# Performance work log

Hardware: AMD Instinct MI355X
Metric: run time of the kernel (lower is better)

The kernel has to match this reference:

```python
import jax, jax.numpy as jnp
import numpy as np

WIN = 7
SIGMA = 1.5
C1 = 0.01 ** 2
C2 = 0.03 ** 2


def _gaussian_window(channels):
    # 1D gaussian, normalized (matches pytorch_ssim.create_window)
    xs = np.arange(WIN, dtype=np.float32)
    g = np.exp(-((xs - WIN // 2) ** 2) / (2.0 * SIGMA ** 2))
    g = g / g.sum()
    w2d = np.outer(g, g).astype(np.float32)  # [7,7], sums to 1
    # depthwise kernel [C,1,7,7] (OIHW with feature_group_count=C)
    return jnp.asarray(np.tile(w2d[None, None], (channels, 1, 1, 1)))


def _dwconv(img, win, channels):
    # img: [N,C,H,W]; 'same' padding for odd window (pad=3)
    return jax.lax.conv_general_dilated(
        img, win, window_strides=(1, 1), padding=[(3, 3), (3, 3)],
        feature_group_count=channels,
        dimension_numbers=('NCHW', 'OIHW', 'NCHW'))


def _ssim(img1, img2):
    C = img1.shape[1]
    win = _gaussian_window(C).astype(img1.dtype)
    mu1 = _dwconv(img1, win, C)
    mu2 = _dwconv(img2, win, C)
    mu1_sq = mu1 * mu1
    mu2_sq = mu2 * mu2
    mu1_mu2 = mu1 * mu2
    sigma1_sq = _dwconv(img1 * img1, win, C) - mu1_sq
    sigma2_sq = _dwconv(img2 * img2, win, C) - mu2_sq
    sigma12 = _dwconv(img1 * img2, win, C) - mu1_mu2
    ssim_map = ((2.0 * mu1_mu2 + C1) * (2.0 * sigma12 + C2)) / (
        (mu1_sq + mu2_sq + C1) * (sigma1_sq + sigma2_sq + C2))
    return jnp.mean(ssim_map)  # size_average=True


def setup_inputs() -> dict:
    key = jax.random.key(0)
    k1, k2 = jax.random.split(key)
    B, T, C, H, W = 8, 8, 3, 256, 256
    x = jax.random.uniform(k1, (B, T, C, H, W), dtype=jnp.float32)
    y = jax.random.uniform(k2, (B, T, C, H, W), dtype=jnp.float32)
    return {"x": x, "y": y}


def reference(x, y):
    # flatten(0,1): [B,T,C,H,W] -> [B*T,C,H,W]
    x2 = x.reshape((-1,) + x.shape[2:])
    y2 = y.reshape((-1,) + y.shape[2:])
    return _ssim(x2, y2)
```

## Files before the change

### kernel.cpp

```cpp
#include <hip/hip_runtime.h>

#define IMG_H 256
#define IMG_W 256
#define TW 64
#define TH 16
#define SC 72

typedef float v2f __attribute__((ext_vector_type(2)));

__device__ __forceinline__ int rotc(int r, int c) { return (c & ~7) | ((c + r) & 7); }

#define G0 0.03663285f
#define G1 0.11128076f
#define G2 0.21674532f
#define G3 0.27068216f

__global__ __launch_bounds__(256) void ssim_tile_kernel(
    const float* __restrict__ x, const float* __restrict__ y,
    float* __restrict__ partial) {
    __shared__ float4 vs[TH][SC];
    __shared__ float  wsum[4];

    const int tid = threadIdx.x;
    const int bx = blockIdx.x, by = blockIdx.y, plane = blockIdx.z;
    const int r0 = by * TH, c0 = bx * TW;
    const size_t base = (size_t)plane * (IMG_H * IMG_W);
    const float g[7] = {G0, G1, G2, G3, G2, G1, G0};

    v2f g2[7];
    #pragma unroll
    for (int d = 0; d < 7; ++d) { g2[d].x = g[d]; g2[d].y = g[d]; }

    const bool fast = ((bx == 1) | (bx == 2)) & (by >= 1) & (by <= 14);

    auto vtask = [&](int a, int c) {
        const int gc = c0 - 4 + c;
        const int rstart = r0 - 3 + 4 * a;

        float xr[10], yr[10];
        if (fast) {
            const float* px = x + base + (size_t)rstart * IMG_W + gc;
            const float* py = y + base + (size_t)rstart * IMG_W + gc;
            #pragma unroll
            for (int t = 0; t < 10; ++t) {
                xr[t] = px[t * IMG_W];
                yr[t] = py[t * IMG_W];
            }
        } else {
            const bool ok_c = ((unsigned)gc < IMG_W);
            const int  gcc  = gc < 0 ? 0 : (gc > IMG_W - 1 ? IMG_W - 1 : gc);
            #pragma unroll
            for (int t = 0; t < 10; ++t) {
                const int gr  = rstart + t;
                const bool ok = ok_c & ((unsigned)gr < IMG_H);
                const int grc = gr < 0 ? 0 : (gr > IMG_H - 1 ? IMG_H - 1 : gr);
                const size_t idx = base + ((size_t)grc << 8) + gcc;
                float xv = x[idx], yv = y[idx];
                xr[t] = ok ? xv : 0.f;
                yr[t] = ok ? yv : 0.f;
            }
        }

        v2f aA[4], aB[4];
        #pragma unroll
        for (int o = 0; o < 4; ++o) { aA[o] = (v2f)0.f; aB[o] = (v2f)0.f; }

        #pragma unroll
        for (int t = 0; t < 10; ++t) {
            const float xv = xr[t], yv = yr[t];
            v2f ina; ina.x = xv; ina.y = yv;
            v2f inb; inb.x = fmaf(xv, xv, yv * yv); inb.y = xv * yv;
            #pragma unroll
            for (int o = 0; o < 4; ++o) {
                const int dy = t - o;
                if (dy >= 0 && dy < 7) {
                    aA[o] = __builtin_elementwise_fma(g2[dy], ina, aA[o]);
                    aB[o] = __builtin_elementwise_fma(g2[dy], inb, aB[o]);
                }
            }
        }
        #pragma unroll
        for (int o = 0; o < 4; ++o) {
            const int R = 4 * a + o;
            vs[R][rotc(R, c)] = make_float4(aA[o].x, aA[o].y, aB[o].x, aB[o].y);
        }
    };

    vtask(tid >> 6, tid & 63);
    if (tid < 32) vtask(tid >> 3, 64 + (tid & 7));

    __syncthreads();

    const int R = 4 * (tid >> 6) + (tid & 3);
    const int m = (tid >> 2) & 15;

    v2f wa[10], wb[10];
    #pragma unroll
    for (int j = 0; j < 10; ++j) {
        float4 w = vs[R][rotc(R, 4 * m + j + 1)];
        wa[j].x = w.x; wa[j].y = w.y;
        wb[j].x = w.z; wb[j].y = w.w;
    }

    const float c1 = 0.01f * 0.01f;
    const float c2 = 0.03f * 0.03f;
    float acc = 0.f;
    #pragma unroll
    for (int o = 0; o < 4; ++o) {
        v2f sab = (v2f)0.f, szw = (v2f)0.f;
        #pragma unroll
        for (int dx = 0; dx < 7; ++dx) {
            sab = __builtin_elementwise_fma(g2[dx], wa[o + dx], sab);
            szw = __builtin_elementwise_fma(g2[dx], wb[o + dx], szw);
        }
        const float sx = sab.x, sy = sab.y, szz = szw.x, sxy2 = szw.y;
        const float mu1s = sx * sx;
        const float mu2s = sy * sy;
        const float mu12 = sx * sy;
        const float s12  = sxy2 - mu12;
        const float ssum = szz - mu1s - mu2s;
        const float num  = fmaf(2.f, mu12, c1) * fmaf(2.f, s12, c2);
        const float den  = (mu1s + mu2s + c1) * (ssum + c2);
        float rcp = __builtin_amdgcn_rcpf(den);
        rcp = rcp * (2.f - den * rcp);
        acc = fmaf(num, rcp, acc);
    }

    #pragma unroll
    for (int off = 32; off > 0; off >>= 1)
        acc += __shfl_down(acc, off, 64);

    const int wave = tid >> 6;
    const int lane = tid & 63;
    if (lane == 0) wsum[wave] = acc;
    __syncthreads();
    if (tid == 0) {
        float t = wsum[0] + wsum[1] + wsum[2] + wsum[3];
        partial[((size_t)blockIdx.z * 64) + blockIdx.y * 4 + blockIdx.x] = t;
    }
}

__global__ __launch_bounds__(1024) void ssim_reduce_kernel(
    const float4* __restrict__ p, float* __restrict__ out,
    int n4, double inv_count) {
    double a = 0.0;
    for (int i = threadIdx.x; i < n4; i += 1024) {
        float4 v = p[i];
        a += (double)v.x + (double)v.y + (double)v.z + (double)v.w;
    }
    #pragma unroll
    for (int off = 32; off > 0; off >>= 1)
        a += __shfl_down(a, off, 64);
    __shared__ double sd[16];
    const int wave = threadIdx.x >> 6;
    const int lane = threadIdx.x & 63;
    if (lane == 0) sd[wave] = a;
    __syncthreads();
    if (threadIdx.x == 0) {
        double t = 0.0;
        #pragma unroll
        for (int w = 0; w < 16; w++) t += sd[w];
        out[0] = (float)(t * inv_count);
    }
}

extern "C" void kernel_launch(void* const* d_in, const int* in_sizes, int n_in,
                              void* d_out, int out_size, void* d_ws, size_t ws_size,
                              hipStream_t stream) {
    const float* x = (const float*)d_in[0];
    const float* y = (const float*)d_in[1];
    float* out = (float*)d_out;
    float* partial = (float*)d_ws;

    const int total = in_sizes[0];
    const int planes = total / (IMG_H * IMG_W);
    const int tiles_r = IMG_H / TH;
    const int tiles_c = IMG_W / TW;
    const int n_partial = planes * tiles_r * tiles_c;

    dim3 grid(tiles_c, tiles_r, planes);
    ssim_tile_kernel<<<grid, dim3(256), 0, stream>>>(x, y, partial);

    ssim_reduce_kernel<<<1, 1024, 0, stream>>>((const float4*)partial, out,
                                               n_partial / 4, 1.0 / (double)total);
}
```

Measured before the change: 45.40 us.

## Process two vertically adjacent row tiles per block to raise memory-level parallelism

Each block now covers two 16-row tiles, stacked vertically, with a double shared-memory buffer. All global loads for both tiles are issued before any vertical convolution runs, so more loads are in flight per thread. The grid is halved, which amortizes per-block setup and halo overhead. In exchange, register and LDS use per block go up, which may lower occupancy, and the total halo loaded is unchanged because the two tiles do not share their halo rows.

```diff
diff --git a/kernel.cpp b/kernel.cpp
--- a/kernel.cpp
+++ b/kernel.cpp
@@ -18,12 +18,15 @@
 __global__ __launch_bounds__(256) void ssim_tile_kernel(
     const float* __restrict__ x, const float* __restrict__ y,
     float* __restrict__ partial) {
-    __shared__ float4 vs[TH][SC];
+    __shared__ float4 vs[2][TH][SC];
     __shared__ float  wsum[4];
 
     const int tid = threadIdx.x;
     const int bx = blockIdx.x, by = blockIdx.y, plane = blockIdx.z;
-    const int r0 = by * TH, c0 = bx * TW;
+    const int by2 = by * 2;
+    const int r0A = by2 * TH;
+    const int r0B = r0A + TH;
+    const int c0 = bx * TW;
     const size_t base = (size_t)plane * (IMG_H * IMG_W);
     const float g[7] = {G0, G1, G2, G3, G2, G1, G0};
 
@@ -31,13 +34,12 @@
     #pragma unroll
     for (int d = 0; d < 7; ++d) { g2[d].x = g[d]; g2[d].y = g[d]; }
 
-    const bool fast = ((bx == 1) | (bx == 2)) & (by >= 1) & (by <= 14);
-
-    auto vtask = [&](int a, int c) {
-        const int gc = c0 - 4 + c;
+    const bool cols_ok = (bx == 1) | (bx == 2);
+    const bool fastA = cols_ok & (by >= 1);
+    const bool fastB = cols_ok & (by <= 6);
+
+    auto vload = [&](int r0, bool fast, int gc, int a, float* xr, float* yr) {
         const int rstart = r0 - 3 + 4 * a;
-
-        float xr[10], yr[10];
         if (fast) {
             const float* px = x + base + (size_t)rstart * IMG_W + gc;
             const float* py = y + base + (size_t)rstart * IMG_W + gc;
@@ -60,11 +62,12 @@
                 yr[t] = ok ? yv : 0.f;
             }
         }
-
+    };
+
+    auto vcompute = [&](int buf, int a, int c, const float* xr, const float* yr) {
         v2f aA[4], aB[4];
         #pragma unroll
         for (int o = 0; o < 4; ++o) { aA[o] = (v2f)0.f; aB[o] = (v2f)0.f; }
-
         #pragma unroll
         for (int t = 0; t < 10; ++t) {
             const float xv = xr[t], yv = yr[t];
@@ -82,48 +85,59 @@
         #pragma unroll
         for (int o = 0; o < 4; ++o) {
             const int R = 4 * a + o;
-            vs[R][rotc(R, c)] = make_float4(aA[o].x, aA[o].y, aB[o].x, aB[o].y);
+            vs[buf][R][rotc(R, c)] = make_float4(aA[o].x, aA[o].y, aB[o].x, aB[o].y);
         }
     };
 
-    vtask(tid >> 6, tid & 63);
-    if (tid < 32) vtask(tid >> 3, 64 + (tid & 7));
+    auto vtask2 = [&](int a, int c) {
+        const int gc = c0 - 4 + c;
+        float xrA[10], yrA[10], xrB[10], yrB[10];
+        vload(r0A, fastA, gc, a, xrA, yrA);
+        vload(r0B, fastB, gc, a, xrB, yrB);
+        vcompute(0, a, c, xrA, yrA);
+        vcompute(1, a, c, xrB, yrB);
+    };
+
+    vtask2(tid >> 6, tid & 63);
+    if (tid < 32) vtask2(tid >> 3, 64 + (tid & 7));
 
     __syncthreads();
 
     const int R = 4 * (tid >> 6) + (tid & 3);
     const int m = (tid >> 2) & 15;
-
-    v2f wa[10], wb[10];
-    #pragma unroll
-    for (int j = 0; j < 10; ++j) {
-        float4 w = vs[R][rotc(R, 4 * m + j + 1)];
-        wa[j].x = w.x; wa[j].y = w.y;
-        wb[j].x = w.z; wb[j].y = w.w;
-    }
-
     const float c1 = 0.01f * 0.01f;
     const float c2 = 0.03f * 0.03f;
+
     float acc = 0.f;
     #pragma unroll
-    for (int o = 0; o < 4; ++o) {
-        v2f sab = (v2f)0.f, szw = (v2f)0.f;
-        #pragma unroll
-        for (int dx = 0; dx < 7; ++dx) {
-            sab = __builtin_elementwise_fma(g2[dx], wa[o + dx], sab);
-            szw = __builtin_elementwise_fma(g2[dx], wb[o + dx], szw);
-        }
-        const float sx = sab.x, sy = sab.y, szz = szw.x, sxy2 = szw.y;
-        const float mu1s = sx * sx;
-        const float mu2s = sy * sy;
-        const float mu12 = sx * sy;
-        const float s12  = sxy2 - mu12;
-        const float ssum = szz - mu1s - mu2s;
-        const float num  = fmaf(2.f, mu12, c1) * fmaf(2.f, s12, c2);
-        const float den  = (mu1s + mu2s + c1) * (ssum + c2);
-        float rcp = __builtin_amdgcn_rcpf(den);
-        rcp = rcp * (2.f - den * rcp);
-        acc = fmaf(num, rcp, acc);
+    for (int buf = 0; buf < 2; ++buf) {
+        v2f wa[10], wb[10];
+        #pragma unroll
+        for (int j = 0; j < 10; ++j) {
+            float4 w = vs[buf][R][rotc(R, 4 * m + j + 1)];
+            wa[j].x = w.x; wa[j].y = w.y;
+            wb[j].x = w.z; wb[j].y = w.w;
+        }
+        #pragma unroll
+        for (int o = 0; o < 4; ++o) {
+            v2f sab = (v2f)0.f, szw = (v2f)0.f;
+            #pragma unroll
+            for (int dx = 0; dx < 7; ++dx) {
+                sab = __builtin_elementwise_fma(g2[dx], wa[o + dx], sab);
+                szw = __builtin_elementwise_fma(g2[dx], wb[o + dx], szw);
+            }
+            const float sx = sab.x, sy = sab.y, szz = szw.x, sxy2 = szw.y;
+            const float mu1s = sx * sx;
+            const float mu2s = sy * sy;
+            const float mu12 = sx * sy;
+            const float s12  = sxy2 - mu12;
+            const float ssum = szz - mu1s - mu2s;
+            const float num  = fmaf(2.f, mu12, c1) * fmaf(2.f, s12, c2);
+            const float den  = (mu1s + mu2s + c1) * (ssum + c2);
+            float rcp = __builtin_amdgcn_rcpf(den);
+            rcp = rcp * (2.f - den * rcp);
+            acc = fmaf(num, rcp, acc);
+        }
     }
 
     #pragma unroll
@@ -136,7 +150,7 @@
     __syncthreads();
     if (tid == 0) {
         float t = wsum[0] + wsum[1] + wsum[2] + wsum[3];
-        partial[((size_t)blockIdx.z * 64) + blockIdx.y * 4 + blockIdx.x] = t;
+        partial[((size_t)plane * 32) + by * 4 + bx] = t;
     }
 }
 
@@ -174,7 +188,7 @@
 
     const int total = in_sizes[0];
     const int planes = total / (IMG_H * IMG_W);
-    const int tiles_r = IMG_H / TH;
+    const int tiles_r = IMG_H / (2 * TH);
     const int tiles_c = IMG_W / TW;
     const int n_partial = planes * tiles_r * tiles_c;
 
```

Result: no change. 45.86 us (+1.0%).
